# Kernel tuning notes

Measured on AMD Instinct MI355X. Metric: run time of the kernel, lower is better.

## Reference

```python
import jax, jax.numpy as jnp
import numpy as np
from jax import lax

FEAT_STRIDE = 16
NMS_THRESH = 0.7
N_PRE = 6000   # test-mode n_test_pre_nms
N_POST = 300   # test-mode n_test_post_nms
MIN_SIZE = 16.0
SCALE = 1.0
RATIOS = (0.5, 1.0, 2.0)
ANCHOR_SCALES = (8, 16, 32)
BASE = 16
N_ANCHOR = len(RATIOS) * len(ANCHOR_SCALES)  # 9


def _anchor_base():
    py = px = BASE / 2.0
    ab = np.zeros((N_ANCHOR, 4), np.float32)
    for i, r in enumerate(RATIOS):
        for j, s in enumerate(ANCHOR_SCALES):
            h = BASE * s * np.sqrt(r)
            w = BASE * s * np.sqrt(1.0 / r)
            k = i * len(ANCHOR_SCALES) + j
            ab[k] = [py - h / 2.0, px - w / 2.0, py + h / 2.0, px + w / 2.0]
    return ab


def _anchors(hh, ww):
    # enumerate_shifted_anchor: (y1,x1,y2,x2) anchors for every feature cell
    ab = _anchor_base()
    sy = np.arange(0, hh * FEAT_STRIDE, FEAT_STRIDE)
    sx = np.arange(0, ww * FEAT_STRIDE, FEAT_STRIDE)
    SX, SY = np.meshgrid(sx, sy)
    shift = np.stack([SY.ravel(), SX.ravel(), SY.ravel(), SX.ravel()], 1)
    anc = (ab[None, :, :] + shift[:, None, :]).reshape(-1, 4).astype(np.float32)
    return jnp.asarray(anc)


def _iou(b):
    # b: [N,4] (y1,x1,y2,x2) -> [N,N] IoU
    y1, x1, y2, x2 = b[:, 0], b[:, 1], b[:, 2], b[:, 3]
    area = (y2 - y1) * (x2 - x1)
    ih = jnp.clip(jnp.minimum(y2[:, None], y2[None, :]) - jnp.maximum(y1[:, None], y1[None, :]), 0.0)
    iw = jnp.clip(jnp.minimum(x2[:, None], x2[None, :]) - jnp.maximum(x1[:, None], x1[None, :]), 0.0)
    inter = ih * iw
    return inter / (area[:, None] + area[None, :] - inter + 1e-9)


def _propose(loc, fg, anchor, img_h, img_w):
    # loc:[M,4] fg:[M] anchor:[M,4]  -> padded [N_POST,4] rois + valid mask
    ah = anchor[:, 2] - anchor[:, 0]
    aw = anchor[:, 3] - anchor[:, 1]
    acy = anchor[:, 0] + 0.5 * ah
    acx = anchor[:, 1] + 0.5 * aw
    cy = loc[:, 0] * ah + acy
    cx = loc[:, 1] * aw + acx
    h = jnp.exp(loc[:, 2]) * ah
    w = jnp.exp(loc[:, 3]) * aw
    roi = jnp.stack([
        jnp.clip(cy - 0.5 * h, 0.0, img_h),
        jnp.clip(cx - 0.5 * w, 0.0, img_w),
        jnp.clip(cy + 0.5 * h, 0.0, img_h),
        jnp.clip(cx + 0.5 * w, 0.0, img_w),
    ], axis=1)
    hs = roi[:, 2] - roi[:, 0]
    ws = roi[:, 3] - roi[:, 1]
    ms = MIN_SIZE * SCALE
    valid = (hs >= ms) & (ws >= ms)
    sc = jnp.where(valid, fg, -jnp.inf)  # drop too-small boxes from ranking
    top_sc, idx = lax.top_k(sc, N_PRE)   # score-sorted pre-NMS candidates
    boxes = roi[idx]
    ok = lax.stop_gradient(jnp.isfinite(top_sc))
    sup = lax.stop_gradient(_iou(boxes) > NMS_THRESH)  # [N_PRE,N_PRE]
    tri = jnp.arange(N_PRE)

    def body(i, keep):
        suppressed = jnp.any(keep & sup[:, i] & (tri < i))
        return keep.at[i].set(ok[i] & ~suppressed)

    keep = lax.fori_loop(0, N_PRE, body, jnp.zeros((N_PRE,), bool))
    rank = jnp.cumsum(keep.astype(jnp.int32)) - 1
    sel = keep & (rank < N_POST)
    tgt = jnp.where(sel, rank, N_POST)  # N_POST is out-of-bounds -> dropped
    out = jnp.zeros((N_POST, 4), boxes.dtype).at[tgt].set(boxes, mode='drop')
    vmask = jnp.zeros((N_POST,), bool).at[tgt].set(True, mode='drop')
    return out, vmask


def reference(x, conv1_w, conv1_b, score_w, score_b, loc_w, loc_b, img_h, img_w):
    n, _, hh, ww = x.shape
    anchor = _anchors(hh, ww)
    h = jax.nn.relu(
        lax.conv_general_dilated(x, conv1_w, (1, 1), 'SAME',
                                 dimension_numbers=('NCHW', 'OIHW', 'NCHW'))
        + conv1_b[None, :, None, None])
    locs = jnp.einsum('nchw,oc->nohw', h, loc_w[:, :, 0, 0]) + loc_b[None, :, None, None]
    scr = jnp.einsum('nchw,oc->nohw', h, score_w[:, :, 0, 0]) + score_b[None, :, None, None]
    rpn_locs = locs.transpose(0, 2, 3, 1).reshape(n, -1, 4)          # [n,M,4]
    scr_t = scr.transpose(0, 2, 3, 1)                                 # [n,hh,ww,2A]
    soft = jax.nn.softmax(scr_t.reshape(n, hh, ww, N_ANCHOR, 2), axis=-1)
    fg = soft[..., 1].reshape(n, -1)                                  # [n,M]
    rpn_scores = scr_t.reshape(n, -1, 2)
    rois, vmask = jax.vmap(lambda l, f: _propose(l, f, anchor, img_h, img_w))(rpn_locs, fg)
    roi_indices = jnp.broadcast_to(jnp.arange(n, dtype=jnp.int32)[:, None], (n, N_POST))
    return rpn_locs, rpn_scores, rois, roi_indices, anchor, vmask


def setup_inputs() -> dict:
    key = jax.random.key(0)
    ks = jax.random.split(key, 4)
    x = jax.random.normal(ks[0], (2, 512, 64, 64), jnp.float32)
    conv1_w = 0.01 * jax.random.normal(ks[1], (512, 512, 3, 3), jnp.float32)
    conv1_b = jnp.zeros((512,), jnp.float32)
    score_w = 0.01 * jax.random.normal(ks[2], (N_ANCHOR * 2, 512, 1, 1), jnp.float32)
    score_b = jnp.zeros((N_ANCHOR * 2,), jnp.float32)
    loc_w = 0.01 * jax.random.normal(ks[3], (N_ANCHOR * 4, 512, 1, 1), jnp.float32)
    loc_b = jnp.zeros((N_ANCHOR * 4,), jnp.float32)
    return {"x": x, "conv1_w": conv1_w, "conv1_b": conv1_b,
            "score_w": score_w, "score_b": score_b,
            "loc_w": loc_w, "loc_b": loc_b,
            "img_h": 1024, "img_w": 1024}
```

## Files before the change

### kernel.cpp

```cpp
#include <hip/hip_runtime.h>
#include <hip/hip_bf16.h>
#include <math.h>
#include <cstdint>

typedef unsigned long long u64;
typedef unsigned int u32;
typedef _Float16 half8 __attribute__((ext_vector_type(8)));
typedef float floatx4 __attribute__((ext_vector_type(4)));

#define NANCH 36864
#define SEG 65536
#define N_PRE 6000
#define N_POST 300
#define NW 96
#define NPADC 6144

#define O0 0
#define O1 294912
#define O2 442368
#define O3 444768
#define O4 445368
#define O5 592824

#define WS_XHI   0
#define WS_XLO   2097152
#define WS_WHI   4194304
#define WS_WLO   5373952
#define WS_WSLT  6553600
#define WS_WSLB  6586368
#define WS_H     6586432
#define WS_GUARD 10780736
#define WS_FG    0
#define WS_ROI   73728
#define WS_KEYS  368640
#define WS_SBOX  630784
#define WS_ALIVE 679936
#define WS_MASK  4194304

#define HSCALE 9.5367431640625e-07f

__device__ __forceinline__ void gl_lds16(const void* g, void* l) {
  __builtin_amdgcn_global_load_lds(
      (const __attribute__((address_space(1))) u32*)g,
      (__attribute__((address_space(3))) u32*)l, 16, 0, 0);
}

__device__ __forceinline__ u64 bcast64(u64 v, int src) {
  u32 lo = (u32)__shfl((int)(v & 0xFFFFFFFFull), src);
  u32 hi = (u32)__shfl((int)(v >> 32), src);
  return ((u64)hi << 32) | lo;
}

__global__ __launch_bounds__(256) void prep_all(
    const float* __restrict__ x, const float* __restrict__ w,
    const float* __restrict__ lw, const float* __restrict__ sw,
    const float* __restrict__ lb, const float* __restrict__ sb,
    float4* __restrict__ h, float4* __restrict__ guard,
    _Float16* __restrict__ xhi, _Float16* __restrict__ xlo,
    _Float16* __restrict__ whi, _Float16* __restrict__ wlo,
    float* __restrict__ wslt, float* __restrict__ wslb) {
  __shared__ float s[64 * 65];
  const int b = blockIdx.x, tid = threadIdx.x;
  if (b < 4097) {
    int idx = b * 256 + tid;
    if (idx < 1048576) h[idx] = make_float4(0.f, 0.f, 0.f, 0.f);
    else if (idx < 1048576 + 16) guard[idx - 1048576] = make_float4(0.f, 0.f, 0.f, 0.f);
    return;
  }
  if (b < 5121) {
    int l = b - 4097;
    int pt = l & 63, cg = (l >> 6) & 7, n = l >> 9;
    const int c0 = cg << 6, p0 = pt << 6;
#pragma unroll
    for (int kk = 0; kk < 16; ++kk) {
      int e = tid + (kk << 8);
      int ci = e >> 6, pi = e & 63;
      s[ci * 65 + pi] = x[(((size_t)(n * 512 + c0 + ci)) << 12) + p0 + pi];
    }
    __syncthreads();
#pragma unroll
    for (int kk = 0; kk < 16; ++kk) {
      int e = tid + (kk << 8);
      int ci = e & 63, pi = e >> 6;
      float sv = s[ci * 65 + pi] * 1024.f;
      _Float16 hi = (_Float16)sv;
      _Float16 lo = (_Float16)(sv - (float)hi);
      size_t off = (((size_t)(n << 12) + p0 + pi) << 9) + c0 + ci;
      xhi[off] = hi;
      xlo[off] = lo;
    }
    return;
  }
  if (b < 5697) {
    int l = b - 5121;
    int ct = l & 7, ot = (l >> 3) & 7, t = l >> 6;
    const int c0 = ct << 6, o0 = ot << 6;
#pragma unroll
    for (int kk = 0; kk < 16; ++kk) {
      int e = tid + (kk << 8);
      int ci = e & 63, oi = e >> 6;
      float sv = w[(size_t)(o0 + oi) * 4608 + (c0 + ci) * 9 + t] * 1024.f;
      _Float16 hi = (_Float16)sv;
      _Float16 lo = (_Float16)(sv - (float)hi);
      size_t off = ((size_t)((t << 9) + o0 + oi) << 9) + c0 + ci;
      whi[off] = hi;
      wlo[off] = lo;
    }
    return;
  }
  {
    int e = (b - 5697) * 256 + tid;
    if (e < 32768) {
      int c = e >> 6, o = e & 63;
      float v = 0.f;
      if (o < 36) v = lw[o * 512 + c];
      else if (o < 54) v = sw[(o - 36) * 512 + c];
      wslt[e] = v;
    } else if (e < 32832) {
      int o = e - 32768;
      float v = 0.f;
      if (o < 36) v = lb[o];
      else if (o < 54) v = sb[o - 36];
      wslb[o] = v;
    }
  }
}

__global__ __launch_bounds__(256) void conv_mfma(
    const _Float16* __restrict__ xhi, const _Float16* __restrict__ xlo,
    const _Float16* __restrict__ whi, const _Float16* __restrict__ wlo,
    const float* __restrict__ guard, float* __restrict__ hout) {
  __shared__ _Float16 aHi[4 * 68 * 32];
  __shared__ _Float16 aLo[4 * 68 * 32];
  __shared__ _Float16 bHi[128 * 32];
  __shared__ _Float16 bLo[128 * 32];
  const int tid = threadIdx.x;
  const int lane = tid & 63, w = tid >> 6;
  const int ptile = blockIdx.x;
  const int og = blockIdx.y;
  const int kq = blockIdx.z;
  const int n = ptile >> 5;
  const int y0 = (ptile & 31) << 1;
  const int o0 = og << 7;
  const int l15 = lane & 15, l16 = lane >> 4;
  const int ry = w >> 1;
  const int wo = (w & 1) << 6;

  floatx4 acc[4][4];
#pragma unroll
  for (int a = 0; a < 4; ++a)
#pragma unroll
    for (int b = 0; b < 4; ++b) acc[a][b] = (floatx4)0.f;

  for (int s = 0; s < 8; ++s) {
    const int c0 = (kq << 8) + (s << 5);
    __syncthreads();
    for (int i = w; i < 17; i += 4) {
      int chunk = (i << 6) + lane;
      int p = chunk >> 2, q = chunk & 3;
      int r = p / 68, xs = p - r * 68;
      int y = y0 - 1 + r, xg = xs - 1;
      bool ok = ((unsigned)y < 64u) && ((unsigned)xg < 64u);
      size_t off = (((size_t)(n << 12) + (y << 6) + xg) << 9) + c0 + (q << 3);
      const void* gh = ok ? (const void*)(xhi + off) : (const void*)guard;
      const void* gl = ok ? (const void*)(xlo + off) : (const void*)guard;
      gl_lds16(gh, (char*)aHi + (i << 10));
      gl_lds16(gl, (char*)aLo + (i << 10));
    }
    for (int tt = 0; tt < 9; ++tt) {
      if (tt > 0) __syncthreads();
      for (int i = w; i < 8; i += 4) {
        int chunk = (i << 6) + lane;
        int row = chunk >> 2, q = chunk & 3;
        size_t off = ((size_t)((tt << 9) + o0 + row) << 9) + c0 + (q << 3);
        gl_lds16((const void*)(whi + off), (char*)bHi + (i << 10));
        gl_lds16((const void*)(wlo + off), (char*)bLo + (i << 10));
      }
      __syncthreads();

      const int dy = tt / 3, dx = tt - 3 * dy;
      half8 ah[4], al[4], bh[4], bl[4];
#pragma unroll
      for (int im = 0; im < 4; ++im) {
        int xp = (im << 4) + l15;
        int p = (ry + dy) * 68 + xp + dx;
        ah[im] = *(const half8*)&aHi[(p << 5) + (l16 << 3)];
        al[im] = *(const half8*)&aLo[(p << 5) + (l16 << 3)];
      }
#pragma unroll
      for (int in = 0; in < 4; ++in) {
        int orow = wo + (in << 4) + l15;
        bh[in] = *(const half8*)&bHi[(orow << 5) + (l16 << 3)];
        bl[in] = *(const half8*)&bLo[(orow << 5) + (l16 << 3)];
      }
#pragma unroll
      for (int im = 0; im < 4; ++im)
#pragma unroll
        for (int in = 0; in < 4; ++in) {
          acc[im][in] = __builtin_amdgcn_mfma_f32_16x16x32_f16(
              ah[im], bh[in], acc[im][in], 0, 0, 0);
          acc[im][in] = __builtin_amdgcn_mfma_f32_16x16x32_f16(
              ah[im], bl[in], acc[im][in], 0, 0, 0);
          acc[im][in] = __builtin_amdgcn_mfma_f32_16x16x32_f16(
              al[im], bh[in], acc[im][in], 0, 0, 0);
        }
    }
  }

#pragma unroll
  for (int im = 0; im < 4; ++im)
#pragma unroll
    for (int in = 0; in < 4; ++in) {
      int o = o0 + wo + (in << 4) + l15;
#pragma unroll
      for (int reg = 0; reg < 4; ++reg) {
        int m_local = (ry << 6) + (im << 4) + (l16 << 2) + reg;
        size_t off = (((size_t)(n << 12) + (y0 << 6) + m_local) << 9) + o;
        atomicAdd(&hout[off], acc[im][in][reg]);
      }
    }
}

__global__ __launch_bounds__(256) void head_kernel(
    const float* __restrict__ hbuf, const float* __restrict__ cb,
    const float* __restrict__ wslt, const float* __restrict__ wslb,
    float* __restrict__ out, float* __restrict__ fgbuf) {
  const int y = blockIdx.x, n = blockIdx.y;
  __shared__ float sH[16 * 65];
  __shared__ float sWt[1024];
  __shared__ float sOut[64 * 65];
  const int tid = threadIdx.x;
  const int x = tid & 63, og = tid >> 6;

  float acc[16];
#pragma unroll
  for (int j = 0; j < 16; ++j) acc[j] = 0.f;

  const float* hb = hbuf + (((size_t)(n << 12) + (y << 6)) << 9);

  for (int c0 = 0; c0 < 512; c0 += 16) {
    __syncthreads();
#pragma unroll
    for (int p = 0; p < 4; ++p) {
      int e = tid + (p << 8);
      {
        int cc = e & 15, xx = e >> 4;
        float raw = hb[((size_t)xx << 9) + c0 + cc];
        sH[cc * 65 + xx] = fmaxf(raw * HSCALE + cb[c0 + cc], 0.f);
      }
      {
        int cc = e >> 6, xx = e & 63;
        sWt[e] = wslt[((c0 + cc) << 6) + xx];
      }
    }
    __syncthreads();
#pragma unroll
    for (int cc = 0; cc < 16; ++cc) {
      float hv = sH[cc * 65 + x];
      const float4* wp = (const float4*)&sWt[(cc << 6) + (og << 4)];
      float4 w0 = wp[0], w1 = wp[1], w2 = wp[2], w3 = wp[3];
      acc[0]  = fmaf(hv, w0.x, acc[0]);  acc[1]  = fmaf(hv, w0.y, acc[1]);
      acc[2]  = fmaf(hv, w0.z, acc[2]);  acc[3]  = fmaf(hv, w0.w, acc[3]);
      acc[4]  = fmaf(hv, w1.x, acc[4]);  acc[5]  = fmaf(hv, w1.y, acc[5]);
      acc[6]  = fmaf(hv, w1.z, acc[6]);  acc[7]  = fmaf(hv, w1.w, acc[7]);
      acc[8]  = fmaf(hv, w2.x, acc[8]);  acc[9]  = fmaf(hv, w2.y, acc[9]);
      acc[10] = fmaf(hv, w2.z, acc[10]); acc[11] = fmaf(hv, w2.w, acc[11]);
      acc[12] = fmaf(hv, w3.x, acc[12]); acc[13] = fmaf(hv, w3.y, acc[13]);
      acc[14] = fmaf(hv, w3.z, acc[14]); acc[15] = fmaf(hv, w3.w, acc[15]);
    }
  }
  __syncthreads();
#pragma unroll
  for (int j = 0; j < 16; ++j) {
    int o = (og << 4) + j;
    sOut[o * 65 + x] = acc[j] + wslb[o];
  }
  __syncthreads();

  const int p0 = (n << 12) + (y << 6);
  float* locs = out + O0 + (size_t)p0 * 36;
  for (int e = tid; e < 2304; e += 256) {
    int xx = e / 36, o = e - xx * 36;
    locs[e] = sOut[o * 65 + xx];
  }
  float* scrs = out + O1 + (size_t)p0 * 18;
  for (int e = tid; e < 1152; e += 256) {
    int xx = e / 18, ss = e - xx * 18;
    scrs[e] = sOut[(36 + ss) * 65 + xx];
  }
  float* fg = fgbuf + n * NANCH + (y << 6) * 9;
  for (int e = tid; e < 576; e += 256) {
    int xx = e / 9, a = e - xx * 9;
    float s0 = sOut[(36 + 2 * a) * 65 + xx];
    float s1 = sOut[(36 + 2 * a + 1) * 65 + xx];
    fg[e] = 1.0f / (1.0f + expf(s0 - s1));
  }
}

__global__ __launch_bounds__(256) void decode_kernel(
    const float* __restrict__ out0, const float* __restrict__ fgbuf,
    float4* __restrict__ roibuf, u64* __restrict__ keys,
    float* __restrict__ anchor_out, float* __restrict__ out,
    const int* __restrict__ imgh_p, const int* __restrict__ imgw_p) {
  int gid = blockIdx.x * 256 + threadIdx.x;
  if (gid < 3600) {
    if (gid < 2400) out[O2 + gid] = 0.f;
    else if (gid < 3000) out[O3 + (gid - 2400)] = (float)((gid - 2400) / 300);
    else out[O5 + (gid - 3000)] = 0.f;
  }
  int n = gid >> 16, k = gid & (SEG - 1);
  if (k >= NANCH) { keys[gid] = ~0ull; return; }
  int a = k % 9;
  int p = k / 9;
  int py = p >> 6, px = p & 63;

  const double R[3] = {0.5, 1.0, 2.0};
  const double S[3] = {8.0, 16.0, 32.0};
  double r = R[a / 3], s = S[a - (a / 3) * 3];
  double hd = 16.0 * s * sqrt(r);
  double wd = 16.0 * s * sqrt(1.0 / r);
  float ay1 = (float)(8.0 - hd / 2.0) + (float)(py * 16);
  float ax1 = (float)(8.0 - wd / 2.0) + (float)(px * 16);
  float ay2 = (float)(8.0 + hd / 2.0) + (float)(py * 16);
  float ax2 = (float)(8.0 + wd / 2.0) + (float)(px * 16);
  if (n == 0) {
    float* ao = anchor_out + (size_t)k * 4;
    ao[0] = ay1; ao[1] = ax1; ao[2] = ay2; ao[3] = ax2;
  }
  float ahk = ay2 - ay1, awk = ax2 - ax1;
  float acy = ay1 + 0.5f * ahk, acx = ax1 + 0.5f * awk;
  const float* lp = out0 + ((size_t)(n * NANCH + k) << 2);
  float dy = lp[0], dx = lp[1], dh = lp[2], dw = lp[3];
  float cy = dy * ahk + acy;
  float cx = dx * awk + acx;
  float bh = expf(dh) * ahk;
  float bw = expf(dw) * awk;
  float img_h = (float)imgh_p[0], img_w = (float)imgw_p[0];
  float y1 = fminf(fmaxf(cy - 0.5f * bh, 0.f), img_h);
  float x1 = fminf(fmaxf(cx - 0.5f * bw, 0.f), img_w);
  float y2 = fminf(fmaxf(cy + 0.5f * bh, 0.f), img_h);
  float x2 = fminf(fmaxf(cx + 0.5f * bw, 0.f), img_w);
  bool valid = ((y2 - y1) >= 16.f) && ((x2 - x1) >= 16.f);
  float sc = valid ? fgbuf[n * NANCH + k] : -INFINITY;
  roibuf[n * NANCH + k] = make_float4(y1, x1, y2, x2);
  unsigned int b = __float_as_uint(sc);
  unsigned int m = b ^ ((b & 0x80000000u) ? 0xFFFFFFFFu : 0x80000000u);
  keys[gid] = ((u64)(~m) << 32) | (unsigned int)k;
}

__global__ __launch_bounds__(256) void sort_local_a(u64* __restrict__ keys) {
  __shared__ u64 sk[4096];
  const int base = blockIdx.x << 12;
  for (int e = threadIdx.x; e < 4096; e += 256) sk[e] = keys[base + e];
  __syncthreads();
  for (int k = 2; k <= 4096; k <<= 1) {
    for (int j = k >> 1; j > 0; j >>= 1) {
      for (int t = threadIdx.x; t < 2048; t += 256) {
        int l = ((t & ~(j - 1)) << 1) | (t & (j - 1));
        int rr = l | j;
        bool asc = (((base + l) & k) == 0);
        u64 a = sk[l], b = sk[rr];
        if ((a > b) == asc) { sk[l] = b; sk[rr] = a; }
      }
      __syncthreads();
    }
  }
  for (int e = threadIdx.x; e < 4096; e += 256) keys[base + e] = sk[e];
}

__global__ __launch_bounds__(256) void sort_global_pass(u64* __restrict__ keys,
                                                        int k, int j) {
  int t = blockIdx.x * 256 + threadIdx.x;
  int l = ((t & ~(j - 1)) << 1) | (t & (j - 1));
  int rr = l | j;
  bool asc = (((l & (SEG - 1)) & k) == 0);
  u64 a = keys[l], b = keys[rr];
  if ((a > b) == asc) { keys[l] = b; keys[rr] = a; }
}

__global__ __launch_bounds__(256) void sort_global_pass2(u64* __restrict__ keys,
                                                         int k, int j1) {
  int t = blockIdx.x * 256 + threadIdx.x;
  int j2 = j1 >> 1;
  int l = ((t & ~(j2 - 1)) << 1) | (t & (j2 - 1));
  l = ((l & ~(j1 - 1)) << 1) | (l & (j1 - 1));
  u64 e0 = keys[l], e1 = keys[l | j2], e2 = keys[l | j1], e3 = keys[l | j1 | j2];
  bool asc = (((l & (SEG - 1)) & k) == 0);
  u64 tmp;
  if ((e0 > e2) == asc) { tmp = e0; e0 = e2; e2 = tmp; }
  if ((e1 > e3) == asc) { tmp = e1; e1 = e3; e3 = tmp; }
  if ((e0 > e1) == asc) { tmp = e0; e0 = e1; e1 = tmp; }
  if ((e2 > e3) == asc) { tmp = e2; e2 = e3; e3 = tmp; }
  keys[l] = e0; keys[l | j2] = e1; keys[l | j1] = e2; keys[l | j1 | j2] = e3;
}

__global__ __launch_bounds__(256) void sort_local_b(u64* __restrict__ keys, int k) {
  __shared__ u64 sk[4096];
  const int base = blockIdx.x << 12;
  for (int e = threadIdx.x; e < 4096; e += 256) sk[e] = keys[base + e];
  __syncthreads();
  for (int j = 2048; j > 0; j >>= 1) {
    for (int t = threadIdx.x; t < 2048; t += 256) {
      int l = ((t & ~(j - 1)) << 1) | (t & (j - 1));
      int rr = l | j;
      bool asc = ((((base + l) & (SEG - 1)) & k) == 0);
      u64 a = sk[l], b = sk[rr];
      if ((a > b) == asc) { sk[l] = b; sk[rr] = a; }
    }
    __syncthreads();
  }
  for (int e = threadIdx.x; e < 4096; e += 256) keys[base + e] = sk[e];
}

__global__ __launch_bounds__(256) void nms_gather(
    const u64* __restrict__ keys, const float4* __restrict__ roibuf,
    float4* __restrict__ sbox, u64* __restrict__ alive) {
  const int n = blockIdx.y;
  int i = blockIdx.x * 256 + threadIdx.x;
  u64 kk = (i < N_PRE) ? keys[(n << 16) + i] : ~0ull;
  bool valid = ((unsigned)(kk >> 32)) < 0xFF800000u;
  float4 b = make_float4(0.f, 0.f, 0.f, 0.f);
  if (valid) b = roibuf[(size_t)n * NANCH + (unsigned)(kk & 0xFFFFFFFFull)];
  sbox[n * NPADC + i] = b;
  u64 bal = __ballot(valid);
  if ((threadIdx.x & 63) == 0) alive[n * NW + (i >> 6)] = bal;
}

__global__ __launch_bounds__(256) void build_mask(
    const float4* __restrict__ sbox, u64* __restrict__ M) {
  __shared__ float4 jb[4][64];
  __shared__ float ja[4][64];
  const int tid = threadIdx.x, lane = tid & 63, wv = tid >> 6;
  const int g = blockIdx.x, q = blockIdx.y, n = blockIdx.z;
  const float4* sb = sbox + n * NPADC;
  float4 bi = sb[(g << 6) + lane];
  float ai = (bi.z - bi.x) * (bi.w - bi.y);
  u64* Mrow = M + ((size_t)(n * NPADC + (g << 6) + lane)) * NW;
#pragma unroll
  for (int it = 0; it < 6; ++it) {
    int w = q * 24 + (it << 2) + wv;
    float4 bjl = sb[(w << 6) + lane];
    jb[wv][lane] = bjl;
    ja[wv][lane] = (bjl.z - bjl.x) * (bjl.w - bjl.y);
    u64 bits = 0;
#pragma unroll 8
    for (int j = 0; j < 64; ++j) {
      float4 bj = jb[wv][j];
      float aj = ja[wv][j];
      float ih = fmaxf(fminf(bi.z, bj.z) - fmaxf(bi.x, bj.x), 0.f);
      float iw = fmaxf(fminf(bi.w, bj.w) - fmaxf(bi.y, bj.y), 0.f);
      float inter = ih * iw;
      bool bit = inter / (ai + aj - inter + 1e-9f) > 0.7f;
      bits |= ((u64)bit) << j;
    }
    Mrow[w] = bits;
  }
}

__global__ __launch_bounds__(64) void nms_reduce(
    const u64* __restrict__ M, const u64* __restrict__ alive,
    const float4* __restrict__ sbox, float* __restrict__ out) {
  const int n = blockIdx.x, lane = threadIdx.x;
  float* rois = out + O2 + n * (N_POST * 4);
  float* vmask = out + O5 + n * N_POST;
  const u64* A = alive + n * NW;
  const u64* Mb = M + (size_t)n * NPADC * NW;
  const float4* sb = sbox + n * NPADC;
  u64 aw0 = A[lane];
  u64 aw1 = (lane < 32) ? A[64 + lane] : 0ull;
  u64 accA = 0, accB = 0;
  int nk = 0;
  u64 dnext = Mb[(size_t)lane * NW + 0];
  float4 bnext = sb[lane];
  const u64 below = lane ? (~0ull >> (64 - lane)) : 0ull;

  for (int c = 0; c < 94; ++c) {
    u64 dcur = dnext;
    float4 bcur = bnext;
    if (c + 1 < 94) {
      dnext = Mb[(size_t)(((c + 1) << 6) + lane) * NW + (c + 1)];
      bnext = sb[((c + 1) << 6) + lane];
    }
    u64 wacc = (c < 64) ? bcast64(accA, c) : bcast64(accB, c - 64);
    u64 aw = (c < 64) ? bcast64(aw0, c) : bcast64(aw1, c - 64);
    u64 alive_u = aw & ~wacc;
    if (alive_u == 0ull) continue;

    u64 dmask = dcur & below;
    u64 rem = alive_u, kept = 0;
    while (rem) {
      int j = __builtin_ctzll(rem);
      kept |= 1ull << j;
      u64 col = __ballot((dmask >> j) & 1);
      rem &= ~(col | (1ull << j));
    }

    int npop = __popcll(kept);
    if ((kept >> lane) & 1ull) {
      int slot = nk + __popcll(kept & below);
      if (slot < N_POST) {
        rois[slot * 4 + 0] = bcur.x; rois[slot * 4 + 1] = bcur.y;
        rois[slot * 4 + 2] = bcur.z; rois[slot * 4 + 3] = bcur.w;
        vmask[slot] = 1.0f;
      }
    }
    if (nk + npop >= N_POST) break;
    nk += npop;

    u64 kk = kept;
    while (kk) {
      int j0 = __builtin_ctzll(kk); kk &= kk - 1;
      int j1 = kk ? __builtin_ctzll(kk) : j0; kk &= kk - 1;
      int j2 = kk ? __builtin_ctzll(kk) : j0; kk &= kk - 1;
      int j3 = kk ? __builtin_ctzll(kk) : j0; kk &= kk - 1;
      int j4 = kk ? __builtin_ctzll(kk) : j0; kk &= kk - 1;
      int j5 = kk ? __builtin_ctzll(kk) : j0; kk &= kk - 1;
      int j6 = kk ? __builtin_ctzll(kk) : j0; kk &= kk - 1;
      int j7 = kk ? __builtin_ctzll(kk) : j0; kk &= kk - 1;
      const u64* r0 = Mb + (size_t)((c << 6) + j0) * NW;
      const u64* r1 = Mb + (size_t)((c << 6) + j1) * NW;
      const u64* r2 = Mb + (size_t)((c << 6) + j2) * NW;
      const u64* r3 = Mb + (size_t)((c << 6) + j3) * NW;
      const u64* r4 = Mb + (size_t)((c << 6) + j4) * NW;
      const u64* r5 = Mb + (size_t)((c << 6) + j5) * NW;
      const u64* r6 = Mb + (size_t)((c << 6) + j6) * NW;
      const u64* r7 = Mb + (size_t)((c << 6) + j7) * NW;
      u64 oA = r0[lane] | r1[lane] | r2[lane] | r3[lane]
             | r4[lane] | r5[lane] | r6[lane] | r7[lane];
      u64 oB = 0;
      if (lane < 32)
        oB = r0[64 + lane] | r1[64 + lane] | r2[64 + lane] | r3[64 + lane]
           | r4[64 + lane] | r5[64 + lane] | r6[64 + lane] | r7[64 + lane];
      accA |= oA;
      accB |= oB;
    }
  }
}

extern "C" void kernel_launch(void* const* d_in, const int* in_sizes, int n_in,
                              void* d_out, int out_size, void* d_ws, size_t ws_size,
                              hipStream_t stream) {
  const float* x        = (const float*)d_in[0];
  const float* conv1_w  = (const float*)d_in[1];
  const float* conv1_b  = (const float*)d_in[2];
  const float* score_w  = (const float*)d_in[3];
  const float* score_b  = (const float*)d_in[4];
  const float* loc_w    = (const float*)d_in[5];
  const float* loc_b    = (const float*)d_in[6];
  const int*   imgh_p   = (const int*)d_in[7];
  const int*   imgw_p   = (const int*)d_in[8];

  float* out = (float*)d_out;
  float* ws  = (float*)d_ws;

  _Float16* xhi = (_Float16*)(ws + WS_XHI);
  _Float16* xlo = (_Float16*)(ws + WS_XLO);
  _Float16* whi = (_Float16*)(ws + WS_WHI);
  _Float16* wlo = (_Float16*)(ws + WS_WLO);
  float* wslt   = ws + WS_WSLT;
  float* wslb   = ws + WS_WSLB;
  float* hbuf   = ws + WS_H;
  float* guard  = ws + WS_GUARD;
  float* fgbuf   = ws + WS_FG;
  float4* roibuf = (float4*)(ws + WS_ROI);
  u64* keys      = (u64*)(ws + WS_KEYS);
  float4* sbox   = (float4*)(ws + WS_SBOX);
  u64* alive     = (u64*)(ws + WS_ALIVE);
  u64* maskbuf   = (u64*)(ws + WS_MASK);

  prep_all<<<5826, 256, 0, stream>>>(x, conv1_w, loc_w, score_w, loc_b, score_b,
                                     (float4*)hbuf, (float4*)guard,
                                     xhi, xlo, whi, wlo, wslt, wslb);

  conv_mfma<<<dim3(64, 4, 2), 256, 0, stream>>>(xhi, xlo, whi, wlo, guard, hbuf);

  head_kernel<<<dim3(64, 2), 256, 0, stream>>>(hbuf, conv1_b, wslt, wslb, out, fgbuf);
  decode_kernel<<<512, 256, 0, stream>>>(out, fgbuf, roibuf, keys,
                                         out + O4, out, imgh_p, imgw_p);

  sort_local_a<<<32, 256, 0, stream>>>(keys);
  for (int k = 8192; k <= SEG; k <<= 1) {
    int j = k >> 1;
    while (j >= 4096) {
      if (j >= 8192) {
        sort_global_pass2<<<128, 256, 0, stream>>>(keys, k, j);
        j >>= 2;
      } else {
        sort_global_pass<<<256, 256, 0, stream>>>(keys, k, j);
        j >>= 1;
      }
    }
    sort_local_b<<<32, 256, 0, stream>>>(keys, k);
  }

  nms_gather<<<dim3(24, 2), 256, 0, stream>>>(keys, roibuf, sbox, alive);
  build_mask<<<dim3(96, 4, 2), 256, 0, stream>>>(sbox, maskbuf);
  nms_reduce<<<2, 64, 0, stream>>>(maskbuf, alive, sbox, out);
}
```

Measured before the change: 501.1 us.

## Replace full bitonic sort with histogram threshold, compaction, and small LDS sort

Replaces the multi-launch global bitonic sort over 64K keys per image with a top-k selection. A 16-bit radix histogram finds the score bucket that holds the 6000th key, candidates at or above that bucket are compacted into an 8192-slot buffer, and a single-block LDS bitonic sort orders them and gathers boxes. This removes many kernel launches and global sort passes. If the threshold bucket overflows the cap, candidates can be dropped, and the order of compacted keys depends on atomics, although the final sort restores a deterministic order.

```diff
diff --git a/kernel.cpp b/kernel.cpp
--- a/kernel.cpp
+++ b/kernel.cpp
@@ -14,6 +14,7 @@
 #define N_POST 300
 #define NW 96
 #define NPADC 6144
+#define CAP 8192
 
 #define O0 0
 #define O1 294912
@@ -35,6 +36,9 @@
 #define WS_KEYS  368640
 #define WS_SBOX  630784
 #define WS_ALIVE 679936
+#define WS_CBUF  680320
+#define WS_HIST  713088
+#define WS_CNT   844160
 #define WS_MASK  4194304
 
 #define HSCALE 9.5367431640625e-07f
@@ -301,15 +305,19 @@
     const float* __restrict__ out0, const float* __restrict__ fgbuf,
     float4* __restrict__ roibuf, u64* __restrict__ keys,
     float* __restrict__ anchor_out, float* __restrict__ out,
+    u32* __restrict__ hist, u64* __restrict__ cbuf, u32* __restrict__ cnt,
     const int* __restrict__ imgh_p, const int* __restrict__ imgw_p) {
   int gid = blockIdx.x * 256 + threadIdx.x;
+  hist[gid] = 0u;
+  if (gid < 2 * CAP) cbuf[gid] = ~0ull;
+  if (gid < 4) cnt[gid] = 0u;
   if (gid < 3600) {
     if (gid < 2400) out[O2 + gid] = 0.f;
     else if (gid < 3000) out[O3 + (gid - 2400)] = (float)((gid - 2400) / 300);
     else out[O5 + (gid - 3000)] = 0.f;
   }
   int n = gid >> 16, k = gid & (SEG - 1);
-  if (k >= NANCH) { keys[gid] = ~0ull; return; }
+  if (k >= NANCH) return;
   int a = k % 9;
   int p = k / 9;
   int py = p >> 6, px = p & 63;
@@ -348,82 +356,91 @@
   keys[gid] = ((u64)(~m) << 32) | (unsigned int)k;
 }
 
-__global__ __launch_bounds__(256) void sort_local_a(u64* __restrict__ keys) {
-  __shared__ u64 sk[4096];
-  const int base = blockIdx.x << 12;
-  for (int e = threadIdx.x; e < 4096; e += 256) sk[e] = keys[base + e];
+__global__ __launch_bounds__(256) void hist_kernel(
+    const u64* __restrict__ keys, u32* __restrict__ hist) {
+  const int n = blockIdx.y;
+  int i = blockIdx.x * 256 + threadIdx.x;
+  u32 hk = (u32)(keys[(n << 16) + i] >> 32);
+  if (hk < 0xFF800000u) atomicAdd(&hist[(n << 16) + (hk >> 16)], 1u);
+}
+
+__global__ __launch_bounds__(1024) void thresh_kernel(
+    const u32* __restrict__ hist, u32* __restrict__ cnt) {
+  const int n = blockIdx.x, t = threadIdx.x;
+  __shared__ u32 sc[1024];
+  const uint4* hp = (const uint4*)(hist + (n << 16));
+  u32 s = 0;
+#pragma unroll
+  for (int q = 0; q < 16; ++q) {
+    uint4 v = hp[t * 16 + q];
+    s += v.x + v.y + v.z + v.w;
+  }
+  sc[t] = s;
   __syncthreads();
-  for (int k = 2; k <= 4096; k <<= 1) {
+  for (int off = 1; off < 1024; off <<= 1) {
+    u32 v = (t >= off) ? sc[t - off] : 0u;
+    __syncthreads();
+    sc[t] += v;
+    __syncthreads();
+  }
+  u32 total = sc[1023];
+  u32 target = total < (u32)N_PRE ? total : (u32)N_PRE;
+  u32 mycum = sc[t];
+  u32 prev = t ? sc[t - 1] : 0u;
+  if (total > 0 && mycum >= target && prev < target) {
+    u32 base = prev;
+    int b = t << 6;
+    while (true) {
+      base += hist[(n << 16) + b];
+      if (base >= target) break;
+      ++b;
+    }
+    cnt[2 + n] = (u32)b;
+  }
+}
+
+__global__ __launch_bounds__(256) void compact_kernel(
+    const u64* __restrict__ keys, u32* __restrict__ cnt,
+    u64* __restrict__ cbuf) {
+  const int n = blockIdx.y;
+  int i = blockIdx.x * 256 + threadIdx.x;
+  u64 key = keys[(n << 16) + i];
+  u32 hk = (u32)(key >> 32);
+  u32 T = cnt[2 + n];
+  if (hk < 0xFF800000u && (hk >> 16) <= T) {
+    u32 slot = atomicAdd(&cnt[n], 1u);
+    if (slot < (u32)CAP) cbuf[(n << 13) + slot] = key;
+  }
+}
+
+__global__ __launch_bounds__(1024) void sortgather_kernel(
+    const u64* __restrict__ cbuf, const float4* __restrict__ roibuf,
+    float4* __restrict__ sbox, u64* __restrict__ alive) {
+  __shared__ u64 sk[CAP];
+  const int n = blockIdx.x, t = threadIdx.x;
+  for (int e = t; e < CAP; e += 1024) sk[e] = cbuf[(n << 13) + e];
+  __syncthreads();
+  for (int k = 2; k <= CAP; k <<= 1) {
     for (int j = k >> 1; j > 0; j >>= 1) {
-      for (int t = threadIdx.x; t < 2048; t += 256) {
-        int l = ((t & ~(j - 1)) << 1) | (t & (j - 1));
+      for (int q = t; q < (CAP >> 1); q += 1024) {
+        int l = ((q & ~(j - 1)) << 1) | (q & (j - 1));
         int rr = l | j;
-        bool asc = (((base + l) & k) == 0);
+        bool asc = ((l & k) == 0);
         u64 a = sk[l], b = sk[rr];
         if ((a > b) == asc) { sk[l] = b; sk[rr] = a; }
       }
       __syncthreads();
     }
   }
-  for (int e = threadIdx.x; e < 4096; e += 256) keys[base + e] = sk[e];
-}
-
-__global__ __launch_bounds__(256) void sort_global_pass(u64* __restrict__ keys,
-                                                        int k, int j) {
-  int t = blockIdx.x * 256 + threadIdx.x;
-  int l = ((t & ~(j - 1)) << 1) | (t & (j - 1));
-  int rr = l | j;
-  bool asc = (((l & (SEG - 1)) & k) == 0);
-  u64 a = keys[l], b = keys[rr];
-  if ((a > b) == asc) { keys[l] = b; keys[rr] = a; }
-}
-
-__global__ __launch_bounds__(256) void sort_global_pass2(u64* __restrict__ keys,
-                                                         int k, int j1) {
-  int t = blockIdx.x * 256 + threadIdx.x;
-  int j2 = j1 >> 1;
-  int l = ((t & ~(j2 - 1)) << 1) | (t & (j2 - 1));
-  l = ((l & ~(j1 - 1)) << 1) | (l & (j1 - 1));
-  u64 e0 = keys[l], e1 = keys[l | j2], e2 = keys[l | j1], e3 = keys[l | j1 | j2];
-  bool asc = (((l & (SEG - 1)) & k) == 0);
-  u64 tmp;
-  if ((e0 > e2) == asc) { tmp = e0; e0 = e2; e2 = tmp; }
-  if ((e1 > e3) == asc) { tmp = e1; e1 = e3; e3 = tmp; }
-  if ((e0 > e1) == asc) { tmp = e0; e0 = e1; e1 = tmp; }
-  if ((e2 > e3) == asc) { tmp = e2; e2 = e3; e3 = tmp; }
-  keys[l] = e0; keys[l | j2] = e1; keys[l | j1] = e2; keys[l | j1 | j2] = e3;
-}
-
-__global__ __launch_bounds__(256) void sort_local_b(u64* __restrict__ keys, int k) {
-  __shared__ u64 sk[4096];
-  const int base = blockIdx.x << 12;
-  for (int e = threadIdx.x; e < 4096; e += 256) sk[e] = keys[base + e];
-  __syncthreads();
-  for (int j = 2048; j > 0; j >>= 1) {
-    for (int t = threadIdx.x; t < 2048; t += 256) {
-      int l = ((t & ~(j - 1)) << 1) | (t & (j - 1));
-      int rr = l | j;
-      bool asc = ((((base + l) & (SEG - 1)) & k) == 0);
-      u64 a = sk[l], b = sk[rr];
-      if ((a > b) == asc) { sk[l] = b; sk[rr] = a; }
-    }
-    __syncthreads();
-  }
-  for (int e = threadIdx.x; e < 4096; e += 256) keys[base + e] = sk[e];
-}
-
-__global__ __launch_bounds__(256) void nms_gather(
-    const u64* __restrict__ keys, const float4* __restrict__ roibuf,
-    float4* __restrict__ sbox, u64* __restrict__ alive) {
-  const int n = blockIdx.y;
-  int i = blockIdx.x * 256 + threadIdx.x;
-  u64 kk = (i < N_PRE) ? keys[(n << 16) + i] : ~0ull;
-  bool valid = ((unsigned)(kk >> 32)) < 0xFF800000u;
-  float4 b = make_float4(0.f, 0.f, 0.f, 0.f);
-  if (valid) b = roibuf[(size_t)n * NANCH + (unsigned)(kk & 0xFFFFFFFFull)];
-  sbox[n * NPADC + i] = b;
-  u64 bal = __ballot(valid);
-  if ((threadIdx.x & 63) == 0) alive[n * NW + (i >> 6)] = bal;
+  for (int i = t; i < NPADC; i += 1024) {
+    u64 kk = sk[i];
+    bool valid = (i < N_PRE) && ((u32)(kk >> 32) < 0xFF800000u);
+    float4 b = make_float4(0.f, 0.f, 0.f, 0.f);
+    if (valid) b = roibuf[(size_t)n * NANCH + (u32)(kk & 0xFFFFFFFFull)];
+    sbox[n * NPADC + i] = b;
+    u64 bal = __ballot(valid);
+    if ((t & 63) == 0) alive[n * NW + (i >> 6)] = bal;
+  }
 }
 
 __global__ __launch_bounds__(256) void build_mask(
@@ -566,6 +583,9 @@
   u64* keys      = (u64*)(ws + WS_KEYS);
   float4* sbox   = (float4*)(ws + WS_SBOX);
   u64* alive     = (u64*)(ws + WS_ALIVE);
+  u64* cbuf      = (u64*)(ws + WS_CBUF);
+  u32* hist      = (u32*)(ws + WS_HIST);
+  u32* cnt       = (u32*)(ws + WS_CNT);
   u64* maskbuf   = (u64*)(ws + WS_MASK);
 
   prep_all<<<5826, 256, 0, stream>>>(x, conv1_w, loc_w, score_w, loc_b, score_b,
@@ -576,24 +596,14 @@
 
   head_kernel<<<dim3(64, 2), 256, 0, stream>>>(hbuf, conv1_b, wslt, wslb, out, fgbuf);
   decode_kernel<<<512, 256, 0, stream>>>(out, fgbuf, roibuf, keys,
-                                         out + O4, out, imgh_p, imgw_p);
-
-  sort_local_a<<<32, 256, 0, stream>>>(keys);
-  for (int k = 8192; k <= SEG; k <<= 1) {
-    int j = k >> 1;
-    while (j >= 4096) {
-      if (j >= 8192) {
-        sort_global_pass2<<<128, 256, 0, stream>>>(keys, k, j);
-        j >>= 2;
-      } else {
-        sort_global_pass<<<256, 256, 0, stream>>>(keys, k, j);
-        j >>= 1;
-      }
-    }
-    sort_local_b<<<32, 256, 0, stream>>>(keys, k);
-  }
-
-  nms_gather<<<dim3(24, 2), 256, 0, stream>>>(keys, roibuf, sbox, alive);
+                                         out + O4, out, hist, cbuf, cnt,
+                                         imgh_p, imgw_p);
+
+  hist_kernel<<<dim3(144, 2), 256, 0, stream>>>(keys, hist);
+  thresh_kernel<<<2, 1024, 0, stream>>>(hist, cnt);
+  compact_kernel<<<dim3(144, 2), 256, 0, stream>>>(keys, cnt, cbuf);
+  sortgather_kernel<<<2, 1024, 0, stream>>>(cbuf, roibuf, sbox, alive);
+
   build_mask<<<dim3(96, 4, 2), 256, 0, stream>>>(sbox, maskbuf);
   nms_reduce<<<2, 64, 0, stream>>>(maskbuf, alive, sbox, out);
 }
```

After: 500.1 us. About the same (-0.2%).
